# Optimization experiments

Hardware: AMD Instinct MI355X
Metric: run time of the kernel (lower is better)

Reference implementation:

```python
import jax, jax.numpy as jnp
import numpy as np

MAX_ITERS = 10


def setup_inputs() -> dict:
    key = jax.random.key(0)
    k1, k2, k3, k4, k5 = jax.random.split(key, 5)
    B, D, H = 8192, 2048, 2048
    s = 1.0 / np.sqrt(H)  # torch default init scale (uniform); we use scaled normal
    return {
        "encoded": jax.random.normal(k1, (B, D), dtype=jnp.float32),
        "w_ih": jax.random.normal(k2, (3 * H, D), dtype=jnp.float32) * s,
        "w_hh": jax.random.normal(k3, (3 * H, H), dtype=jnp.float32) * s,
        "b_ih": jax.random.normal(k4, (3 * H,), dtype=jnp.float32) * s,
        "b_hh": jax.random.normal(k5, (3 * H,), dtype=jnp.float32) * s,
    }


def reference(encoded, w_ih, w_hh, b_ih, b_hh):
    """Iterative GRUCell recurrence (training-mode: full max_iters, no early exit).

    PyTorch GRUCell math:
      r = sigmoid(W_ir x + b_ir + W_hr h + b_hr)
      z = sigmoid(W_iz x + b_iz + W_hz h + b_hz)
      n = tanh(W_in x + b_in + r * (W_hn h + b_hn))
      h' = (1 - z) * n + z * h
    """
    H = w_hh.shape[1]
    # Input projection is constant across iterations (gru_input never changes).
    gi = encoded @ w_ih.T + b_ih  # [B, 3H]
    gi_r, gi_z, gi_n = gi[:, :H], gi[:, H:2 * H], gi[:, 2 * H:]

    def step(h, _):
        gh = h @ w_hh.T + b_hh  # [B, 3H]
        gh_r, gh_z, gh_n = gh[:, :H], gh[:, H:2 * H], gh[:, 2 * H:]
        r = jax.nn.sigmoid(gi_r + gh_r)
        z = jax.nn.sigmoid(gi_z + gh_z)
        n = jnp.tanh(gi_n + r * gh_n)
        h_next = (1.0 - z) * n + z * h
        return h_next, None

    h0 = jnp.zeros((encoded.shape[0], H), dtype=encoded.dtype)
    h, _ = jax.lax.scan(step, h0, None, length=MAX_ITERS)
    return h
```

## Files before the change

### kernel.cpp

```cpp
#include <hip/hip_runtime.h>

typedef _Float16 f16_t;
typedef _Float16 f16x4 __attribute__((ext_vector_type(4)));
typedef _Float16 f16x8 __attribute__((ext_vector_type(8)));
typedef float floatx4 __attribute__((ext_vector_type(4)));

#define GLDS16(gptr, lptr) __builtin_amdgcn_global_load_lds( \
    (const __attribute__((address_space(1))) void*)(gptr),   \
    (__attribute__((address_space(3))) void*)(lptr), 16, 0, 0)

__device__ __forceinline__ float sigmoidf_fast(float x) {
    return 1.f / (1.f + __expf(-x));
}
__device__ __forceinline__ float tanhf_fast(float x) {
    float e = __expf(2.f * x);
    return 1.f - 2.f / (e + 1.f);
}

#define GATE_STRIDE 16777216L

__global__ __launch_bounds__(256)
void cvt_f32_f16(const float* __restrict__ in, f16_t* __restrict__ out, long n)
{
    long i = ((long)blockIdx.x * 256 + threadIdx.x) * 8;
    if (i >= n) return;
    floatx4 a = *(const floatx4*)(in + i);
    floatx4 b = *(const floatx4*)(in + i + 4);
    f16x8 o;
    o[0] = (f16_t)a[0]; o[1] = (f16_t)a[1]; o[2] = (f16_t)a[2]; o[3] = (f16_t)a[3];
    o[4] = (f16_t)b[0]; o[5] = (f16_t)b[1]; o[6] = (f16_t)b[2]; o[7] = (f16_t)b[3];
    *(f16x8*)(out + i) = o;
}

__device__ __forceinline__ void stage_gi(const f16_t* __restrict__ A,
                                         const f16_t* __restrict__ W,
                                         f16_t* Asb, f16_t* Wsb,
                                         int m0, int n0, int k0,
                                         int wave, int srow, int skc)
{
    const int K = 2048;
    #pragma unroll
    for (int j = 0; j < 2; ++j) {
        int c = j * 4 + wave;
        int row = c * 16 + srow;
        GLDS16(A + (size_t)(m0 + row) * K + k0 + skc, Asb + c * 512);
    }
    #pragma unroll
    for (int j = 0; j < 2; ++j) {
        int c = j * 4 + wave;
        int row = c * 16 + srow;
        GLDS16(W + (size_t)(n0 + row) * K + k0 + skc, Wsb + c * 512);
    }
}

__global__ __launch_bounds__(256, 2)
void gemm_gi(const f16_t* __restrict__ A,
             const f16_t* __restrict__ W,
             const float* __restrict__ bias,
             f16_t* __restrict__ giF)
{
    __shared__ __align__(16) f16_t smem[2 * 8192];
    const int tid  = threadIdx.x;
    const int lane = tid & 63;
    const int wave = tid >> 6;
    const int m0 = blockIdx.x * 128;
    const int n0 = blockIdx.y * 128;
    const int wm = (wave >> 1) * 64;
    const int wn = (wave & 1) * 64;

    floatx4 acc[4][4] = {};

    const int srow = lane >> 2;
    const int skc  = (((lane & 3) ^ ((srow >> 1) & 3))) * 8;
    const int fr = lane & 15;
    const int jq = lane >> 4;
    const int jsw = (jq ^ ((fr >> 1) & 3)) * 8;

    stage_gi(A, W, smem, smem + 4096, m0, n0, 0, wave, srow, skc);
    __syncthreads();

    for (int t = 0; t < 64; ++t) {
        f16_t* As = smem + (t & 1) * 8192;
        f16_t* Ws = As + 4096;
        if (t < 63) {
            f16_t* Asn = smem + ((t + 1) & 1) * 8192;
            stage_gi(A, W, Asn, Asn + 4096, m0, n0, (t + 1) * 32,
                     wave, srow, skc);
        }

        f16x8 a_frag[4], b_frag[4];
        #pragma unroll
        for (int u = 0; u < 4; ++u)
            a_frag[u] = *(const f16x8*)(As + (wm + u * 16 + fr) * 32 + jsw);
        #pragma unroll
        for (int u = 0; u < 4; ++u)
            b_frag[u] = *(const f16x8*)(Ws + (wn + u * 16 + fr) * 32 + jsw);
        #pragma unroll
        for (int tm = 0; tm < 4; ++tm)
            #pragma unroll
            for (int tn = 0; tn < 4; ++tn)
                acc[tm][tn] = __builtin_amdgcn_mfma_f32_16x16x32_f16(
                    a_frag[tm], b_frag[tn], acc[tm][tn], 0, 0, 0);
        __syncthreads();
    }

    const int g   = n0 >> 11;
    const int tNb = ((n0 & 2047) >> 4) + (wn >> 4);
    #pragma unroll
    for (int tm = 0; tm < 4; ++tm) {
        int tM = (m0 + wm + tm * 16) >> 4;
        #pragma unroll
        for (int tn = 0; tn < 4; ++tn) {
            int tN = tNb + tn;
            int n  = n0 + wn + tn * 16 + fr;
            float b = bias[n];
            f16x4 v;
            #pragma unroll
            for (int r = 0; r < 4; ++r) v[r] = (f16_t)(acc[tm][tn][r] + b);
            *(f16x4*)(giF + ((size_t)(g * 512 + tM) * 128 + tN) * 256 + lane * 4) = v;
        }
    }
}

__global__ __launch_bounds__(256)
void gru_init(const f16_t* __restrict__ giF,
              const float* __restrict__ bhh,
              f16_t* __restrict__ h16)
{
    const int H = 2048;
    __shared__ __align__(16) f16_t hp[128 * 72];
    const int tid  = threadIdx.x;
    const int lane = tid & 63;
    const int wave = tid >> 6;
    const int m0 = blockIdx.x * 128;
    const int n0 = blockIdx.y * 64;
    const int wm = (wave >> 1) * 64;
    const int wn = (wave & 1) * 32;
    const int colL = lane & 15;
    const int rq = (lane >> 4) * 4;

    #pragma unroll
    for (int tm = 0; tm < 4; ++tm) {
        int tM = (m0 + wm + tm * 16) >> 4;
        #pragma unroll
        for (int tn = 0; tn < 2; ++tn) {
            int tN = ((n0 + wn) >> 4) + tn;
            size_t base = ((size_t)tM * 128 + tN) * 256 + lane * 4;
            f16x4 g_r = *(const f16x4*)(giF + base);
            f16x4 g_z = *(const f16x4*)(giF + base + GATE_STRIDE);
            f16x4 g_n = *(const f16x4*)(giF + base + 2 * GATE_STRIDE);
            int n = n0 + wn + tn * 16 + colL;
            float br = bhh[n], bz = bhh[H + n], bn = bhh[2 * H + n];
            #pragma unroll
            for (int r = 0; r < 4; ++r) {
                float rr = sigmoidf_fast((float)g_r[r] + br);
                float zz = sigmoidf_fast((float)g_z[r] + bz);
                float nn = tanhf_fast((float)g_n[r] + rr * bn);
                float h = (1.f - zz) * nn;
                hp[(wm + tm * 16 + rq + r) * 72 + wn + tn * 16 + colL] = (f16_t)h;
            }
        }
    }
    __syncthreads();
    #pragma unroll
    for (int i = 0; i < 4; ++i) {
        int r2 = i * 32 + (tid >> 3);
        int ch = tid & 7;
        f16x8 v = *(const f16x8*)(hp + r2 * 72 + ch * 8);
        *(f16x8*)(h16 + (size_t)(m0 + r2) * H + n0 + ch * 8) = v;
    }
}

__device__ __forceinline__ void stage_gru(const f16_t* __restrict__ hin,
                                          const f16_t* __restrict__ Wh,
                                          f16_t* Asb, f16_t* Wsb,
                                          int m0, int n0, int kk,
                                          int wave, int srow8, int sgk)
{
    const int K = 2048, H = 2048;
    #pragma unroll
    for (int j = 0; j < 4; ++j) {
        int c = j * 4 + wave;
        int row = c * 8 + srow8;
        GLDS16(hin + (size_t)(m0 + row) * K + kk + sgk, Asb + c * 512);
    }
    #pragma unroll
    for (int j = 0; j < 6; ++j) {
        int c = j * 4 + wave;
        int g = c >> 3;
        int cw = c & 7;
        int row = cw * 8 + srow8;
        GLDS16(Wh + (size_t)(g * H + n0 + row) * K + kk + sgk,
               Wsb + c * 512);
    }
}

__global__ __launch_bounds__(256, 2)
void gru_step(const f16_t* __restrict__ Wh,
              const float* __restrict__ bhh,
              const f16_t* __restrict__ giF,
              const f16_t* __restrict__ hin,
              f16_t* __restrict__ hout,
              float* __restrict__ out32)
{
    const int H = 2048;
    __shared__ __align__(16) f16_t smem[2 * 20480];
    const int tid  = threadIdx.x;
    const int lane = tid & 63;
    const int wave = tid >> 6;

    const int bid   = blockIdx.x;
    const int xcd   = bid & 7;
    const int rblk  = bid >> 3;
    const int m0 = (rblk >> 2) * 128;
    const int n0 = (xcd * 4 + (rblk & 3)) * 64;

    const int wm = (wave >> 1) * 64;
    const int wn = (wave & 1) * 32;

    floatx4 acc[3][4][2] = {};

    const int srow8 = lane >> 3;
    const int sgk   = ((lane & 7) ^ srow8) * 8;
    const int fr = lane & 15;
    const int jq = lane >> 4;
    const int rq = (lane >> 4) * 4;

    f16x4 hold16[4][2];

    stage_gru(hin, Wh, smem, smem + 8192, m0, n0, 0, wave, srow8, sgk);
    __syncthreads();

    for (int t = 0; t < 32; ++t) {
        const int k0 = t * 64;
        f16_t* As  = smem + (t & 1) * 20480;
        f16_t* Wsm = As + 8192;
        if (t < 31) {
            f16_t* Asn = smem + ((t + 1) & 1) * 20480;
            stage_gru(hin, Wh, Asn, Asn + 8192, m0, n0, k0 + 64,
                      wave, srow8, sgk);
        }

        if (k0 == n0) {
            #pragma unroll
            for (int tm = 0; tm < 4; ++tm) {
                #pragma unroll
                for (int tn = 0; tn < 2; ++tn) {
                    #pragma unroll
                    for (int r = 0; r < 4; ++r) {
                        int row_a = wm + tm * 16 + rq + r;
                        int kloc  = wn + tn * 16 + fr;
                        int slot  = (kloc >> 3) ^ (row_a & 7);
                        hold16[tm][tn][r] =
                            As[row_a * 64 + slot * 8 + (kloc & 7)];
                    }
                }
            }
        }

        #pragma unroll
        for (int ksub = 0; ksub < 2; ++ksub) {
            f16x8 a_frag[4];
            #pragma unroll
            for (int u = 0; u < 4; ++u) {
                int row = wm + u * 16 + fr;
                int slot = (ksub * 4 + jq) ^ (row & 7);
                a_frag[u] = *(const f16x8*)(As + row * 64 + slot * 8);
            }
            #pragma unroll
            for (int g = 0; g < 3; ++g) {
                #pragma unroll
                for (int tn = 0; tn < 2; ++tn) {
                    int row_w = wn + tn * 16 + fr;
                    int slot = (ksub * 4 + jq) ^ (row_w & 7);
                    f16x8 b_frag = *(const f16x8*)(Wsm + g * 4096 +
                                                   row_w * 64 + slot * 8);
                    #pragma unroll
                    for (int tm = 0; tm < 4; ++tm)
                        acc[g][tm][tn] = __builtin_amdgcn_mfma_f32_16x16x32_f16(
                            a_frag[tm], b_frag, acc[g][tm][tn], 0, 0, 0);
                }
            }
        }
        __syncthreads();
    }

    f16x4 hv[4][2];
    #pragma unroll
    for (int tm = 0; tm < 4; ++tm) {
        int tM = (m0 + wm + tm * 16) >> 4;
        #pragma unroll
        for (int tn = 0; tn < 2; ++tn) {
            int tN = ((n0 + wn) >> 4) + tn;
            size_t base = ((size_t)tM * 128 + tN) * 256 + lane * 4;
            f16x4 g_r = *(const f16x4*)(giF + base);
            f16x4 g_z = *(const f16x4*)(giF + base + GATE_STRIDE);
            f16x4 g_n = *(const f16x4*)(giF + base + 2 * GATE_STRIDE);
            int n = n0 + wn + tn * 16 + fr;
            float br = bhh[n], bz = bhh[H + n], bn = bhh[2 * H + n];
            #pragma unroll
            for (int r = 0; r < 4; ++r) {
                int m = m0 + wm + tm * 16 + rq + r;
                float rr = sigmoidf_fast((float)g_r[r] + acc[0][tm][tn][r] + br);
                float zz = sigmoidf_fast((float)g_z[r] + acc[1][tm][tn][r] + bz);
                float nn = tanhf_fast((float)g_n[r] +
                                      rr * (acc[2][tm][tn][r] + bn));
                float hold = (float)hold16[tm][tn][r];
                float hnew = (1.f - zz) * nn + zz * hold;
                hv[tm][tn][r] = (f16_t)hnew;
                if (out32) out32[(size_t)m * H + n] = hnew;
            }
        }
    }

    if (!out32) {
        f16_t* hp = smem;
        #pragma unroll
        for (int tm = 0; tm < 4; ++tm)
            #pragma unroll
            for (int tn = 0; tn < 2; ++tn)
                #pragma unroll
                for (int r = 0; r < 4; ++r)
                    hp[(wm + tm * 16 + rq + r) * 72 + wn + tn * 16 + fr] =
                        hv[tm][tn][r];
        __syncthreads();
        #pragma unroll
        for (int i = 0; i < 4; ++i) {
            int r2 = i * 32 + (tid >> 3);
            int ch = tid & 7;
            f16x8 v = *(const f16x8*)(hp + r2 * 72 + ch * 8);
            *(f16x8*)(hout + (size_t)(m0 + r2) * H + n0 + ch * 8) = v;
        }
    }
}

extern "C" void kernel_launch(void* const* d_in, const int* in_sizes, int n_in,
                              void* d_out, int out_size, void* d_ws, size_t ws_size,
                              hipStream_t stream) {
    const float* x    = (const float*)d_in[0];
    const float* w_ih = (const float*)d_in[1];
    const float* w_hh = (const float*)d_in[2];
    const float* b_ih = (const float*)d_in[3];
    const float* b_hh = (const float*)d_in[4];
    float* out = (float*)d_out;

    char* ws = (char*)d_ws;
    f16_t* xh    = (f16_t*)(ws);
    f16_t* wih_h = (f16_t*)(ws + 33554432);
    f16_t* whh_h = (f16_t*)(ws + 33554432 + 25165824);
    f16_t* gi    = (f16_t*)(ws + 33554432 + 2 * 25165824);
    f16_t* h16a  = (f16_t*)(ws + 33554432 + 2 * 25165824 + 100663296);
    f16_t* h16b  = (f16_t*)(ws + 33554432 + 2 * 25165824 + 100663296 + 33554432);

    cvt_f32_f16<<<dim3(8192), 256, 0, stream>>>(x, xh, 16777216L);
    cvt_f32_f16<<<dim3(6144), 256, 0, stream>>>(w_ih, wih_h, 12582912L);
    cvt_f32_f16<<<dim3(6144), 256, 0, stream>>>(w_hh, whh_h, 12582912L);

    gemm_gi<<<dim3(64, 48), 256, 0, stream>>>(xh, wih_h, b_ih, gi);
    gru_init<<<dim3(64, 32), 256, 0, stream>>>(gi, b_hh, h16a);

    f16_t* hin = h16a; f16_t* hout = h16b;
    for (int it = 2; it <= 10; ++it) {
        float* o32 = (it == 10) ? out : nullptr;
        gru_step<<<dim3(2048), 256, 0, stream>>>(whh_h, b_hh, gi,
                                                 hin, hout, o32);
        f16_t* t = hin; hin = hout; hout = t;
    }
}
```

Baseline: 2.364 ms.

## Restructure GRU step into 512-thread 256-row tiles with interleaved staged pipeline

Doubles the block tile from 128 to 256 rows using 8 waves per block with one block per CU, so each staged W tile is reused across more rows. The K loop is split into three phases that interleave LDS fragment loads, MFMA bursts under raised priority, and asynchronous global-to-LDS prefetch of the next W and the A tile two steps ahead, using explicit barriers and vmcnt waits. This aims to cut global traffic for W and hide load latency behind MFMAs, at the risk of lower occupancy and fragile hand-written synchronisation.

Result: slower. 2.547 ms (+7.8%).

```diff
diff --git a/kernel.cpp b/kernel.cpp
--- a/kernel.cpp
+++ b/kernel.cpp
@@ -8,6 +8,10 @@
 #define GLDS16(gptr, lptr) __builtin_amdgcn_global_load_lds( \
     (const __attribute__((address_space(1))) void*)(gptr),   \
     (__attribute__((address_space(3))) void*)(lptr), 16, 0, 0)
+
+#define SBAR()  asm volatile("s_barrier" ::: "memory")
+#define LGKM0() do { asm volatile("s_waitcnt lgkmcnt(0)" ::: "memory"); \
+                     __builtin_amdgcn_sched_barrier(0); } while (0)
 
 __device__ __forceinline__ float sigmoidf_fast(float x) {
     return 1.f / (1.f + __expf(-x));
@@ -171,31 +175,34 @@
     }
 }
 
-__device__ __forceinline__ void stage_gru(const f16_t* __restrict__ hin,
-                                          const f16_t* __restrict__ Wh,
-                                          f16_t* Asb, f16_t* Wsb,
-                                          int m0, int n0, int kk,
-                                          int wave, int srow8, int sgk)
-{
-    const int K = 2048, H = 2048;
+__device__ __forceinline__ void stage_A8(const f16_t* __restrict__ hin,
+                                         f16_t* Asb, int m0, int kk,
+                                         int wave, int srow8, int sgk)
+{
+    const int K = 2048;
     #pragma unroll
     for (int j = 0; j < 4; ++j) {
-        int c = j * 4 + wave;
+        int c = j * 8 + wave;
         int row = c * 8 + srow8;
         GLDS16(hin + (size_t)(m0 + row) * K + kk + sgk, Asb + c * 512);
     }
-    #pragma unroll
-    for (int j = 0; j < 6; ++j) {
-        int c = j * 4 + wave;
+}
+__device__ __forceinline__ void stage_W8(const f16_t* __restrict__ Wh,
+                                         f16_t* Wsb, int n0, int kk,
+                                         int wave, int srow8, int sgk)
+{
+    const int K = 2048, H = 2048;
+    #pragma unroll
+    for (int j = 0; j < 3; ++j) {
+        int c = j * 8 + wave;
         int g = c >> 3;
         int cw = c & 7;
         int row = cw * 8 + srow8;
-        GLDS16(Wh + (size_t)(g * H + n0 + row) * K + kk + sgk,
-               Wsb + c * 512);
-    }
-}
-
-__global__ __launch_bounds__(256, 2)
+        GLDS16(Wh + (size_t)(g * H + n0 + row) * K + kk + sgk, Wsb + c * 512);
+    }
+}
+
+__global__ __launch_bounds__(512, 1)
 void gru_step(const f16_t* __restrict__ Wh,
               const float* __restrict__ bhh,
               const f16_t* __restrict__ giF,
@@ -204,7 +211,9 @@
               float* __restrict__ out32)
 {
     const int H = 2048;
-    __shared__ __align__(16) f16_t smem[2 * 20480];
+    __shared__ __align__(16) f16_t smem[2 * 16384 + 2 * 12288];
+    f16_t* smA = smem;
+    f16_t* smW = smem + 32768;
     const int tid  = threadIdx.x;
     const int lane = tid & 63;
     const int wave = tid >> 6;
@@ -212,7 +221,7 @@
     const int bid   = blockIdx.x;
     const int xcd   = bid & 7;
     const int rblk  = bid >> 3;
-    const int m0 = (rblk >> 2) * 128;
+    const int m0 = (rblk >> 2) * 256;
     const int n0 = (xcd * 4 + (rblk & 3)) * 64;
 
     const int wm = (wave >> 1) * 64;
@@ -228,18 +237,40 @@
 
     f16x4 hold16[4][2];
 
-    stage_gru(hin, Wh, smem, smem + 8192, m0, n0, 0, wave, srow8, sgk);
-    __syncthreads();
+#define LOADA(dst, s) do {                                               \
+    _Pragma("unroll")                                                    \
+    for (int u = 0; u < 4; ++u) {                                        \
+        int row = wm + u * 16 + fr;                                      \
+        int slot = ((s) * 4 + jq) ^ (row & 7);                           \
+        dst[u] = *(const f16x8*)(As + row * 64 + slot * 8);              \
+    } } while (0)
+#define LOADB(dst, g, s) do {                                            \
+    _Pragma("unroll")                                                    \
+    for (int tn = 0; tn < 2; ++tn) {                                     \
+        int row_w = wn + tn * 16 + fr;                                   \
+        int slot = ((s) * 4 + jq) ^ (row_w & 7);                         \
+        dst[tn] = *(const f16x8*)(Ws + (g) * 4096 + row_w * 64 + slot * 8); \
+    } } while (0)
+#define MFMA8(g, af, bf) do {                                            \
+    _Pragma("unroll")                                                    \
+    for (int tn = 0; tn < 2; ++tn)                                       \
+        _Pragma("unroll")                                                \
+        for (int tm = 0; tm < 4; ++tm)                                   \
+            acc[g][tm][tn] = __builtin_amdgcn_mfma_f32_16x16x32_f16(     \
+                af[tm], bf[tn], acc[g][tm][tn], 0, 0, 0);                \
+    } while (0)
+
+    stage_A8(hin, smA, m0, 0, wave, srow8, sgk);
+    stage_W8(Wh, smW, n0, 0, wave, srow8, sgk);
+    stage_A8(hin, smA + 16384, m0, 64, wave, srow8, sgk);
+    asm volatile("s_waitcnt vmcnt(4)" ::: "memory");
+    SBAR();
 
     for (int t = 0; t < 32; ++t) {
-        const int k0 = t * 64;
-        f16_t* As  = smem + (t & 1) * 20480;
-        f16_t* Wsm = As + 8192;
-        if (t < 31) {
-            f16_t* Asn = smem + ((t + 1) & 1) * 20480;
-            stage_gru(hin, Wh, Asn, Asn + 8192, m0, n0, k0 + 64,
-                      wave, srow8, sgk);
-        }
+        const int k0 = t << 6;
+        f16_t* As = smA + (t & 1) * 16384;
+        f16_t* Ws = smW + (t & 1) * 12288;
+        f16_t* Wn = smW + ((t + 1) & 1) * 12288;
 
         if (k0 == n0) {
             #pragma unroll
@@ -258,31 +289,47 @@
             }
         }
 
-        #pragma unroll
-        for (int ksub = 0; ksub < 2; ++ksub) {
-            f16x8 a_frag[4];
-            #pragma unroll
-            for (int u = 0; u < 4; ++u) {
-                int row = wm + u * 16 + fr;
-                int slot = (ksub * 4 + jq) ^ (row & 7);
-                a_frag[u] = *(const f16x8*)(As + row * 64 + slot * 8);
-            }
-            #pragma unroll
-            for (int g = 0; g < 3; ++g) {
-                #pragma unroll
-                for (int tn = 0; tn < 2; ++tn) {
-                    int row_w = wn + tn * 16 + fr;
-                    int slot = (ksub * 4 + jq) ^ (row_w & 7);
-                    f16x8 b_frag = *(const f16x8*)(Wsm + g * 4096 +
-                                                   row_w * 64 + slot * 8);
-                    #pragma unroll
-                    for (int tm = 0; tm < 4; ++tm)
-                        acc[g][tm][tn] = __builtin_amdgcn_mfma_f32_16x16x32_f16(
-                            a_frag[tm], b_frag, acc[g][tm][tn], 0, 0, 0);
-                }
-            }
-        }
-        __syncthreads();
+        f16x8 aS0[4], aS1[4], bA[2], bB[2];
+
+        LOADA(aS0, 0);
+        LOADB(bA, 0, 0);
+        LOADB(bB, 1, 0);
+        if (t < 31) stage_W8(Wh, Wn, n0, k0 + 64, wave, srow8, sgk);
+        SBAR();
+        LGKM0();
+        __builtin_amdgcn_s_setprio(1);
+        MFMA8(0, aS0, bA);
+        MFMA8(1, aS0, bB);
+        __builtin_amdgcn_s_setprio(0);
+        SBAR();
+
+        LOADA(aS1, 1);
+        LOADB(bA, 2, 0);
+        LOADB(bB, 0, 1);
+        SBAR();
+        LGKM0();
+        __builtin_amdgcn_s_setprio(1);
+        MFMA8(2, aS0, bA);
+        MFMA8(0, aS1, bB);
+        __builtin_amdgcn_s_setprio(0);
+        SBAR();
+
+        LOADB(bA, 1, 1);
+        LOADB(bB, 2, 1);
+        if (t < 30) stage_A8(hin, As, m0, k0 + 128, wave, srow8, sgk);
+        SBAR();
+        LGKM0();
+        __builtin_amdgcn_s_setprio(1);
+        MFMA8(1, aS1, bA);
+        MFMA8(2, aS1, bB);
+        __builtin_amdgcn_s_setprio(0);
+        SBAR();
+
+        if (t < 31) {
+            if (t < 30) asm volatile("s_waitcnt vmcnt(4)" ::: "memory");
+            else        asm volatile("s_waitcnt vmcnt(0)" ::: "memory");
+            SBAR();
+        }
     }
 
     f16x4 hv[4][2];
@@ -326,12 +373,15 @@
         __syncthreads();
         #pragma unroll
         for (int i = 0; i < 4; ++i) {
-            int r2 = i * 32 + (tid >> 3);
+            int r2 = i * 64 + (tid >> 3);
             int ch = tid & 7;
             f16x8 v = *(const f16x8*)(hp + r2 * 72 + ch * 8);
             *(f16x8*)(hout + (size_t)(m0 + r2) * H + n0 + ch * 8) = v;
         }
     }
+#undef LOADA
+#undef LOADB
+#undef MFMA8
 }
 
 extern "C" void kernel_launch(void* const* d_in, const int* in_sizes, int n_in,
@@ -362,7 +412,7 @@
     f16_t* hin = h16a; f16_t* hout = h16b;
     for (int it = 2; it <= 10; ++it) {
         float* o32 = (it == 10) ? out : nullptr;
-        gru_step<<<dim3(2048), 256, 0, stream>>>(whh_h, b_hh, gi,
+        gru_step<<<dim3(1024), 512, 0, stream>>>(whh_h, b_hh, gi,
                                                  hin, hout, o32);
         f16_t* t = hin; hin = hout; hout = t;
     }
```

## Restructure input-projection GEMM to reuse gru_step's 3-gate 128x64 tiling and staging

Applied to the files above, without the earlier changes.

The gi GEMM moves from 128x128 tiles with K=32 steps to the same tiling as gru_step. Each block now computes a 128-row by 64-column tile across all three gates, with K=64 steps, XOR-swizzled LDS and an XCD-aware block-to-column mapping. The staging helper is shared between both kernels. The aim is more MFMA work per LDS stage, better A-tile reuse across the three gates, and better L2 locality per XCD, at the cost of more LDS per block and possibly lower occupancy.

Result: faster. 2.314 ms (-2.1%).

```diff
diff --git a/kernel.cpp b/kernel.cpp
--- a/kernel.cpp
+++ b/kernel.cpp
@@ -32,24 +32,27 @@
     *(f16x8*)(out + i) = o;
 }
 
-__device__ __forceinline__ void stage_gi(const f16_t* __restrict__ A,
-                                         const f16_t* __restrict__ W,
+__device__ __forceinline__ void stage_AW(const f16_t* __restrict__ Asrc,
+                                         const f16_t* __restrict__ Wsrc,
                                          f16_t* Asb, f16_t* Wsb,
-                                         int m0, int n0, int k0,
-                                         int wave, int srow, int skc)
-{
-    const int K = 2048;
-    #pragma unroll
-    for (int j = 0; j < 2; ++j) {
+                                         int m0, int n0, int kk,
+                                         int wave, int srow8, int sgk)
+{
+    const int K = 2048, H = 2048;
+    #pragma unroll
+    for (int j = 0; j < 4; ++j) {
         int c = j * 4 + wave;
-        int row = c * 16 + srow;
-        GLDS16(A + (size_t)(m0 + row) * K + k0 + skc, Asb + c * 512);
-    }
-    #pragma unroll
-    for (int j = 0; j < 2; ++j) {
+        int row = c * 8 + srow8;
+        GLDS16(Asrc + (size_t)(m0 + row) * K + kk + sgk, Asb + c * 512);
+    }
+    #pragma unroll
+    for (int j = 0; j < 6; ++j) {
         int c = j * 4 + wave;
-        int row = c * 16 + srow;
-        GLDS16(W + (size_t)(n0 + row) * K + k0 + skc, Wsb + c * 512);
+        int g = c >> 3;
+        int cw = c & 7;
+        int row = cw * 8 + srow8;
+        GLDS16(Wsrc + (size_t)(g * H + n0 + row) * K + kk + sgk,
+               Wsb + c * 512);
     }
 }
 
@@ -59,65 +62,84 @@
              const float* __restrict__ bias,
              f16_t* __restrict__ giF)
 {
-    __shared__ __align__(16) f16_t smem[2 * 8192];
+    const int H = 2048;
+    __shared__ __align__(16) f16_t smem[2 * 20480];
     const int tid  = threadIdx.x;
     const int lane = tid & 63;
     const int wave = tid >> 6;
-    const int m0 = blockIdx.x * 128;
-    const int n0 = blockIdx.y * 128;
+
+    const int bid   = blockIdx.x;
+    const int xcd   = bid & 7;
+    const int rblk  = bid >> 3;
+    const int m0 = (rblk >> 2) * 128;
+    const int n0 = (xcd * 4 + (rblk & 3)) * 64;
+
     const int wm = (wave >> 1) * 64;
-    const int wn = (wave & 1) * 64;
-
-    floatx4 acc[4][4] = {};
-
-    const int srow = lane >> 2;
-    const int skc  = (((lane & 3) ^ ((srow >> 1) & 3))) * 8;
+    const int wn = (wave & 1) * 32;
+
+    floatx4 acc[3][4][2] = {};
+
+    const int srow8 = lane >> 3;
+    const int sgk   = ((lane & 7) ^ srow8) * 8;
     const int fr = lane & 15;
     const int jq = lane >> 4;
-    const int jsw = (jq ^ ((fr >> 1) & 3)) * 8;
-
-    stage_gi(A, W, smem, smem + 4096, m0, n0, 0, wave, srow, skc);
+    const int rq = (lane >> 4) * 4;
+
+    stage_AW(A, W, smem, smem + 8192, m0, n0, 0, wave, srow8, sgk);
     __syncthreads();
 
-    for (int t = 0; t < 64; ++t) {
-        f16_t* As = smem + (t & 1) * 8192;
-        f16_t* Ws = As + 4096;
-        if (t < 63) {
-            f16_t* Asn = smem + ((t + 1) & 1) * 8192;
-            stage_gi(A, W, Asn, Asn + 4096, m0, n0, (t + 1) * 32,
-                     wave, srow, skc);
-        }
-
-        f16x8 a_frag[4], b_frag[4];
-        #pragma unroll
-        for (int u = 0; u < 4; ++u)
-            a_frag[u] = *(const f16x8*)(As + (wm + u * 16 + fr) * 32 + jsw);
-        #pragma unroll
-        for (int u = 0; u < 4; ++u)
-            b_frag[u] = *(const f16x8*)(Ws + (wn + u * 16 + fr) * 32 + jsw);
-        #pragma unroll
-        for (int tm = 0; tm < 4; ++tm)
-            #pragma unroll
-            for (int tn = 0; tn < 4; ++tn)
-                acc[tm][tn] = __builtin_amdgcn_mfma_f32_16x16x32_f16(
-                    a_frag[tm], b_frag[tn], acc[tm][tn], 0, 0, 0);
+    for (int t = 0; t < 32; ++t) {
+        f16_t* As  = smem + (t & 1) * 20480;
+        f16_t* Wsm = As + 8192;
+        if (t < 31) {
+            f16_t* Asn = smem + ((t + 1) & 1) * 20480;
+            stage_AW(A, W, Asn, Asn + 8192, m0, n0, (t + 1) * 64,
+                     wave, srow8, sgk);
+        }
+
+        #pragma unroll
+        for (int ksub = 0; ksub < 2; ++ksub) {
+            f16x8 a_frag[4];
+            #pragma unroll
+            for (int u = 0; u < 4; ++u) {
+                int row = wm + u * 16 + fr;
+                int slot = (ksub * 4 + jq) ^ (row & 7);
+                a_frag[u] = *(const f16x8*)(As + row * 64 + slot * 8);
+            }
+            #pragma unroll
+            for (int g = 0; g < 3; ++g) {
+                #pragma unroll
+                for (int tn = 0; tn < 2; ++tn) {
+                    int row_w = wn + tn * 16 + fr;
+                    int slot = (ksub * 4 + jq) ^ (row_w & 7);
+                    f16x8 b_frag = *(const f16x8*)(Wsm + g * 4096 +
+                                                   row_w * 64 + slot * 8);
+                    #pragma unroll
+                    for (int tm = 0; tm < 4; ++tm)
+                        acc[g][tm][tn] = __builtin_amdgcn_mfma_f32_16x16x32_f16(
+                            a_frag[tm], b_frag, acc[g][tm][tn], 0, 0, 0);
+                }
+            }
+        }
         __syncthreads();
     }
 
-    const int g   = n0 >> 11;
-    const int tNb = ((n0 & 2047) >> 4) + (wn >> 4);
     #pragma unroll
     for (int tm = 0; tm < 4; ++tm) {
         int tM = (m0 + wm + tm * 16) >> 4;
         #pragma unroll
-        for (int tn = 0; tn < 4; ++tn) {
-            int tN = tNb + tn;
+        for (int tn = 0; tn < 2; ++tn) {
+            int tN = ((n0 + wn) >> 4) + tn;
             int n  = n0 + wn + tn * 16 + fr;
-            float b = bias[n];
-            f16x4 v;
-            #pragma unroll
-            for (int r = 0; r < 4; ++r) v[r] = (f16_t)(acc[tm][tn][r] + b);
-            *(f16x4*)(giF + ((size_t)(g * 512 + tM) * 128 + tN) * 256 + lane * 4) = v;
+            #pragma unroll
+            for (int g = 0; g < 3; ++g) {
+                float b = bias[g * H + n];
+                f16x4 v;
+                #pragma unroll
+                for (int r = 0; r < 4; ++r) v[r] = (f16_t)(acc[g][tm][tn][r] + b);
+                *(f16x4*)(giF + ((size_t)(g * 512 + tM) * 128 + tN) * 256 +
+                          lane * 4) = v;
+            }
         }
     }
 }
@@ -171,30 +193,6 @@
     }
 }
 
-__device__ __forceinline__ void stage_gru(const f16_t* __restrict__ hin,
-                                          const f16_t* __restrict__ Wh,
-                                          f16_t* Asb, f16_t* Wsb,
-                                          int m0, int n0, int kk,
-                                          int wave, int srow8, int sgk)
-{
-    const int K = 2048, H = 2048;
-    #pragma unroll
-    for (int j = 0; j < 4; ++j) {
-        int c = j * 4 + wave;
-        int row = c * 8 + srow8;
-        GLDS16(hin + (size_t)(m0 + row) * K + kk + sgk, Asb + c * 512);
-    }
-    #pragma unroll
-    for (int j = 0; j < 6; ++j) {
-        int c = j * 4 + wave;
-        int g = c >> 3;
-        int cw = c & 7;
-        int row = cw * 8 + srow8;
-        GLDS16(Wh + (size_t)(g * H + n0 + row) * K + kk + sgk,
-               Wsb + c * 512);
-    }
-}
-
 __global__ __launch_bounds__(256, 2)
 void gru_step(const f16_t* __restrict__ Wh,
               const float* __restrict__ bhh,
@@ -228,7 +226,7 @@
 
     f16x4 hold16[4][2];
 
-    stage_gru(hin, Wh, smem, smem + 8192, m0, n0, 0, wave, srow8, sgk);
+    stage_AW(hin, Wh, smem, smem + 8192, m0, n0, 0, wave, srow8, sgk);
     __syncthreads();
 
     for (int t = 0; t < 32; ++t) {
@@ -237,8 +235,8 @@
         f16_t* Wsm = As + 8192;
         if (t < 31) {
             f16_t* Asn = smem + ((t + 1) & 1) * 20480;
-            stage_gru(hin, Wh, Asn, Asn + 8192, m0, n0, k0 + 64,
-                      wave, srow8, sgk);
+            stage_AW(hin, Wh, Asn, Asn + 8192, m0, n0, k0 + 64,
+                     wave, srow8, sgk);
         }
 
         if (k0 == n0) {
@@ -356,7 +354,7 @@
     cvt_f32_f16<<<dim3(6144), 256, 0, stream>>>(w_ih, wih_h, 12582912L);
     cvt_f32_f16<<<dim3(6144), 256, 0, stream>>>(w_hh, whh_h, 12582912L);
 
-    gemm_gi<<<dim3(64, 48), 256, 0, stream>>>(xh, wih_h, b_ih, gi);
+    gemm_gi<<<dim3(2048), 256, 0, stream>>>(xh, wih_h, b_ih, gi);
     gru_init<<<dim3(64, 32), 256, 0, stream>>>(gi, b_hh, h16a);
 
     f16_t* hin = h16a; f16_t* hout = h16b;
```
